# Optimization experiments

Hardware: AMD Instinct MI355X
Metric: run time of the kernel (lower is better)

## Reference

```python
import jax, jax.numpy as jnp
import numpy as np

VOCAB, HIDDEN, BATCH, SEQ = 50000, 256, 64, 2048


def setup_inputs() -> dict:
    key = jax.random.key(0)
    k1, k2, k3, k4 = jax.random.split(key, 4)
    embed = jax.random.normal(k1, (VOCAB, HIDDEN), dtype=jnp.float32) * 0.02
    embed = embed.at[0].set(0.0)  # padding_idx=0
    # orthogonal-ish init approximated by scaled normal; values irrelevant for correctness
    W_x_w = jax.random.normal(k2, (HIDDEN, HIDDEN), dtype=jnp.float32) / np.sqrt(HIDDEN)
    W_x_b = jnp.zeros((HIDDEN,), dtype=jnp.float32)
    W_h_w = jax.random.normal(k3, (HIDDEN, HIDDEN), dtype=jnp.float32) / np.sqrt(HIDDEN)
    x = jax.random.randint(k4, (BATCH, SEQ), 0, VOCAB)
    return {"x": x, "embed": embed, "W_x_w": W_x_w, "W_x_b": W_x_b, "W_h_w": W_h_w}


def reference(x, embed, W_x_w, W_x_b, W_h_w):
    # input projection precomputed for all timesteps: [B, S, H]
    inp = embed[x]                                  # embedding lookup (dropout p=0 is identity)
    x_pre = jnp.einsum('bsd,hd->bsh', inp, W_x_w) + W_x_b
    Wh_t = W_h_w.T                                  # matches torch.mm(h, W_h.weight.t())
    h0 = jnp.zeros((x.shape[0], W_h_w.shape[0]), dtype=x_pre.dtype)

    def step(h, xt):                                # xt: [B, H]
        h = jnp.tanh(xt + h @ Wh_t)
        return h, h

    _, all_states = jax.lax.scan(step, h0, jnp.swapaxes(x_pre, 0, 1))  # [S, B, H]
    return jnp.swapaxes(all_states, 0, 1)           # [B, S, H] (return_all_states=True)
```

## Files before the change

### kernel.cpp

```cpp
#include <hip/hip_runtime.h>
#include <hip/hip_bf16.h>

#define HIDDEN 256
#define BATCH  64
#define SEQ    2048

__global__ __launch_bounds__(256, 4)
void xpre_kernel(const int* __restrict__ x,
                 const float* __restrict__ embed,
                 const float* __restrict__ Wx,
                 const float* __restrict__ bias,
                 float* __restrict__ out) {
    const int tid = threadIdx.x;
    const long row0 = (long)blockIdx.x * 32;

    __shared__ int toks[32];
    if (tid < 32) toks[tid] = x[row0 + tid];
    __syncthreads();

    const float* erow[32];
    #pragma unroll
    for (int r = 0; r < 32; ++r) {
        const int tok = __builtin_amdgcn_readfirstlane(toks[r]);
        erow[r] = embed + (size_t)tok * HIDDEN;
    }

    float acc[32];
    const float bj = bias[tid];
    #pragma unroll
    for (int r = 0; r < 32; ++r) acc[r] = bj;

    const float* wrow = Wx + (size_t)tid * HIDDEN;

    #pragma unroll 4
    for (int d0 = 0; d0 < HIDDEN; d0 += 4) {
        const float4 w = *(const float4*)(wrow + d0);
        #pragma unroll
        for (int r = 0; r < 32; ++r) {
            const float4 ev = *(const float4*)(erow[r] + d0);
            float a = acc[r];
            a = fmaf(w.x, ev.x, a);
            a = fmaf(w.y, ev.y, a);
            a = fmaf(w.z, ev.z, a);
            a = fmaf(w.w, ev.w, a);
            acc[r] = a;
        }
    }

    #pragma unroll
    for (int r = 0; r < 32; ++r) {
        out[(row0 + r) * HIDDEN + tid] = acc[r];
    }
}


#define MAC_ASM(RD) \
  "ds_read_b128 v[48:51], " RD "\n\t" \
  "ds_read_b128 v[52:55], " RD " offset:16\n\t" \
  "ds_read_b128 v[56:59], " RD " offset:32\n\t" \
  "ds_read_b128 v[60:63], " RD " offset:48\n\t" \
  "s_waitcnt lgkmcnt(3)\n\t" \
  "v_pk_mul_f32 v[64:65], v[128:129], v[48:49]\n\t" \
  "v_pk_mul_f32 v[66:67], v[144:145], v[48:49]\n\t" \
  "v_pk_mul_f32 v[68:69], v[160:161], v[48:49]\n\t" \
  "v_pk_mul_f32 v[70:71], v[176:177], v[48:49]\n\t" \
  "v_pk_mul_f32 v[72:73], v[192:193], v[48:49]\n\t" \
  "v_pk_mul_f32 v[74:75], v[208:209], v[48:49]\n\t" \
  "v_pk_mul_f32 v[76:77], v[224:225], v[48:49]\n\t" \
  "v_pk_mul_f32 v[78:79], v[240:241], v[48:49]\n\t" \
  "v_pk_fma_f32 v[64:65], v[130:131], v[50:51], v[64:65]\n\t" \
  "v_pk_fma_f32 v[66:67], v[146:147], v[50:51], v[66:67]\n\t" \
  "v_pk_fma_f32 v[68:69], v[162:163], v[50:51], v[68:69]\n\t" \
  "v_pk_fma_f32 v[70:71], v[178:179], v[50:51], v[70:71]\n\t" \
  "v_pk_fma_f32 v[72:73], v[194:195], v[50:51], v[72:73]\n\t" \
  "v_pk_fma_f32 v[74:75], v[210:211], v[50:51], v[74:75]\n\t" \
  "v_pk_fma_f32 v[76:77], v[226:227], v[50:51], v[76:77]\n\t" \
  "v_pk_fma_f32 v[78:79], v[242:243], v[50:51], v[78:79]\n\t" \
  "s_waitcnt lgkmcnt(2)\n\t" \
  "v_pk_fma_f32 v[64:65], v[132:133], v[52:53], v[64:65]\n\t" \
  "v_pk_fma_f32 v[66:67], v[148:149], v[52:53], v[66:67]\n\t" \
  "v_pk_fma_f32 v[68:69], v[164:165], v[52:53], v[68:69]\n\t" \
  "v_pk_fma_f32 v[70:71], v[180:181], v[52:53], v[70:71]\n\t" \
  "v_pk_fma_f32 v[72:73], v[196:197], v[52:53], v[72:73]\n\t" \
  "v_pk_fma_f32 v[74:75], v[212:213], v[52:53], v[74:75]\n\t" \
  "v_pk_fma_f32 v[76:77], v[228:229], v[52:53], v[76:77]\n\t" \
  "v_pk_fma_f32 v[78:79], v[244:245], v[52:53], v[78:79]\n\t" \
  "v_pk_fma_f32 v[64:65], v[134:135], v[54:55], v[64:65]\n\t" \
  "v_pk_fma_f32 v[66:67], v[150:151], v[54:55], v[66:67]\n\t" \
  "v_pk_fma_f32 v[68:69], v[166:167], v[54:55], v[68:69]\n\t" \
  "v_pk_fma_f32 v[70:71], v[182:183], v[54:55], v[70:71]\n\t" \
  "v_pk_fma_f32 v[72:73], v[198:199], v[54:55], v[72:73]\n\t" \
  "v_pk_fma_f32 v[74:75], v[214:215], v[54:55], v[74:75]\n\t" \
  "v_pk_fma_f32 v[76:77], v[230:231], v[54:55], v[76:77]\n\t" \
  "v_pk_fma_f32 v[78:79], v[246:247], v[54:55], v[78:79]\n\t" \
  "s_waitcnt lgkmcnt(1)\n\t" \
  "v_pk_fma_f32 v[64:65], v[136:137], v[56:57], v[64:65]\n\t" \
  "v_pk_fma_f32 v[66:67], v[152:153], v[56:57], v[66:67]\n\t" \
  "v_pk_fma_f32 v[68:69], v[168:169], v[56:57], v[68:69]\n\t" \
  "v_pk_fma_f32 v[70:71], v[184:185], v[56:57], v[70:71]\n\t" \
  "v_pk_fma_f32 v[72:73], v[200:201], v[56:57], v[72:73]\n\t" \
  "v_pk_fma_f32 v[74:75], v[216:217], v[56:57], v[74:75]\n\t" \
  "v_pk_fma_f32 v[76:77], v[232:233], v[56:57], v[76:77]\n\t" \
  "v_pk_fma_f32 v[78:79], v[248:249], v[56:57], v[78:79]\n\t" \
  "v_pk_fma_f32 v[64:65], v[138:139], v[58:59], v[64:65]\n\t" \
  "v_pk_fma_f32 v[66:67], v[154:155], v[58:59], v[66:67]\n\t" \
  "v_pk_fma_f32 v[68:69], v[170:171], v[58:59], v[68:69]\n\t" \
  "v_pk_fma_f32 v[70:71], v[186:187], v[58:59], v[70:71]\n\t" \
  "v_pk_fma_f32 v[72:73], v[202:203], v[58:59], v[72:73]\n\t" \
  "v_pk_fma_f32 v[74:75], v[218:219], v[58:59], v[74:75]\n\t" \
  "v_pk_fma_f32 v[76:77], v[234:235], v[58:59], v[76:77]\n\t" \
  "v_pk_fma_f32 v[78:79], v[250:251], v[58:59], v[78:79]\n\t" \
  "s_waitcnt lgkmcnt(0)\n\t" \
  "v_pk_fma_f32 v[64:65], v[140:141], v[60:61], v[64:65]\n\t" \
  "v_pk_fma_f32 v[66:67], v[156:157], v[60:61], v[66:67]\n\t" \
  "v_pk_fma_f32 v[68:69], v[172:173], v[60:61], v[68:69]\n\t" \
  "v_pk_fma_f32 v[70:71], v[188:189], v[60:61], v[70:71]\n\t" \
  "v_pk_fma_f32 v[72:73], v[204:205], v[60:61], v[72:73]\n\t" \
  "v_pk_fma_f32 v[74:75], v[220:221], v[60:61], v[74:75]\n\t" \
  "v_pk_fma_f32 v[76:77], v[236:237], v[60:61], v[76:77]\n\t" \
  "v_pk_fma_f32 v[78:79], v[252:253], v[60:61], v[78:79]\n\t" \
  "v_pk_fma_f32 v[64:65], v[142:143], v[62:63], v[64:65]\n\t" \
  "v_pk_fma_f32 v[66:67], v[158:159], v[62:63], v[66:67]\n\t" \
  "v_pk_fma_f32 v[68:69], v[174:175], v[62:63], v[68:69]\n\t" \
  "v_pk_fma_f32 v[70:71], v[190:191], v[62:63], v[70:71]\n\t" \
  "v_pk_fma_f32 v[72:73], v[206:207], v[62:63], v[72:73]\n\t" \
  "v_pk_fma_f32 v[74:75], v[222:223], v[62:63], v[74:75]\n\t" \
  "v_pk_fma_f32 v[76:77], v[238:239], v[62:63], v[76:77]\n\t" \
  "v_pk_fma_f32 v[78:79], v[254:255], v[62:63], v[78:79]\n\t" \
  "v_add_f32 v80, v64, v65\n\t" \
  "v_add_f32 v81, v66, v67\n\t" \
  "v_add_f32 v82, v68, v69\n\t" \
  "v_add_f32 v83, v70, v71\n\t" \
  "v_add_f32 v84, v72, v73\n\t" \
  "v_add_f32 v85, v74, v75\n\t" \
  "v_add_f32 v86, v76, v77\n\t" \
  "v_add_f32 v87, v78, v79\n\t"

#define RED_ASM \
  "v_add_f32_dpp v80, v80, v80 row_ror:8 row_mask:0xf bank_mask:0xf\n\t" \
  "v_add_f32_dpp v81, v81, v81 row_ror:8 row_mask:0xf bank_mask:0xf\n\t" \
  "v_add_f32_dpp v82, v82, v82 row_ror:8 row_mask:0xf bank_mask:0xf\n\t" \
  "v_add_f32_dpp v83, v83, v83 row_ror:8 row_mask:0xf bank_mask:0xf\n\t" \
  "v_add_f32_dpp v84, v84, v84 row_ror:8 row_mask:0xf bank_mask:0xf\n\t" \
  "v_add_f32_dpp v85, v85, v85 row_ror:8 row_mask:0xf bank_mask:0xf\n\t" \
  "v_add_f32_dpp v86, v86, v86 row_ror:8 row_mask:0xf bank_mask:0xf\n\t" \
  "v_add_f32_dpp v87, v87, v87 row_ror:8 row_mask:0xf bank_mask:0xf\n\t" \
  "v_cndmask_b32 v88, v81, v80, s[24:25]\n\t" \
  "v_cndmask_b32 v89, v83, v82, s[24:25]\n\t" \
  "v_cndmask_b32 v90, v85, v84, s[24:25]\n\t" \
  "v_cndmask_b32 v91, v87, v86, s[24:25]\n\t" \
  "v_cndmask_b32 v80, v80, v81, s[24:25]\n\t" \
  "v_cndmask_b32 v82, v82, v83, s[24:25]\n\t" \
  "v_cndmask_b32 v84, v84, v85, s[24:25]\n\t" \
  "v_cndmask_b32 v86, v86, v87, s[24:25]\n\t" \
  "v_add_f32_dpp v80, v88, v80 quad_perm:[1,0,3,2] row_mask:0xf bank_mask:0xf\n\t" \
  "v_add_f32_dpp v82, v89, v82 quad_perm:[1,0,3,2] row_mask:0xf bank_mask:0xf\n\t" \
  "v_add_f32_dpp v84, v90, v84 quad_perm:[1,0,3,2] row_mask:0xf bank_mask:0xf\n\t" \
  "v_add_f32_dpp v86, v91, v86 quad_perm:[1,0,3,2] row_mask:0xf bank_mask:0xf\n\t" \
  "v_cndmask_b32 v88, v82, v80, s[26:27]\n\t" \
  "v_cndmask_b32 v89, v86, v84, s[26:27]\n\t" \
  "v_cndmask_b32 v80, v80, v82, s[26:27]\n\t" \
  "v_cndmask_b32 v84, v84, v86, s[26:27]\n\t" \
  "s_nop 1\n\t" \
  "v_add_f32_dpp v80, v88, v80 quad_perm:[2,3,0,1] row_mask:0xf bank_mask:0xf\n\t" \
  "v_add_f32_dpp v84, v89, v84 quad_perm:[2,3,0,1] row_mask:0xf bank_mask:0xf\n\t" \
  "v_cndmask_b32 v88, v84, v80, s[28:29]\n\t" \
  "v_cndmask_b32 v80, v80, v84, s[28:29]\n\t" \
  "s_nop 1\n\t" \
  "v_add_f32_dpp v80, v88, v80 row_ror:4 row_mask:0xf bank_mask:0xf\n\t"

#define FIN_ASM(WR, XP, MD, MS) \
  "s_waitcnt vmcnt(2)\n\t" \
  "v_add_f32 v99, v80, " XP "\n\t" \
  "v_mul_f32 v93, 0x4038AA3B, v99\n\t" \
  "v_exp_f32 v94, v93\n\t" \
  "s_nop 0\n\t" \
  "v_add_f32 v94, 1.0, v94\n\t" \
  "v_rcp_f32 v95, v94\n\t" \
  "s_nop 0\n\t" \
  "v_fma_f32 v99, -2.0, v95, v96\n\t" \
  "s_and_saveexec_b64 s[20:21], s[22:23]\n\t" \
  "ds_write_b32 " WR ", v99\n\t" \
  "global_store_dword v[100:101], v99, off offset:-2048\n\t" \
  "s_mov_b64 exec, s[20:21]\n\t" \
  "v_mov_b32 " MD ", " MS "\n\t" \
  "v_add_co_u32 v100, vcc, 0x400, v100\n\t" \
  "v_addc_co_u32 v101, vcc, v101, 0, vcc\n\t" \
  "s_waitcnt lgkmcnt(0)\n\t" \
  "s_barrier\n\t"

__global__ __attribute__((amdgpu_flat_work_group_size(512, 512)))
void rnn_scan_kernel(const float* __restrict__ Wh,
                     float* __restrict__ out) {
    const int tid = threadIdx.x;
    const int o   = tid & 15;
    const int pc  = tid >> 4;
    const int b   = blockIdx.x;

    __shared__ __align__(16) float hraw[1024];
    hraw[tid] = 0.0f; hraw[tid + 512] = 0.0f;
    __syncthreads();

    unsigned lbase = (unsigned)(unsigned long long)
                     (__attribute__((address_space(3))) char*)hraw;
    const int col  = pc + 32 * (o & 7);
    const int slot = col + 4 * (col >> 4);
    const unsigned rda = lbase + 80u * (unsigned)o;
    const unsigned rdb = rda + 2048u;
    const unsigned wra = lbase + 2048u + 4u * (unsigned)slot;
    const unsigned wrb = wra - 2048u;

    const float* xa = out + ((size_t)b * SEQ + 2) * HIDDEN + col;
    const unsigned xlo = (unsigned)(size_t)xa;
    const unsigned xhi = (unsigned)((size_t)xa >> 32);

    const float* wp0 = Wh + (size_t)(pc +   0) * HIDDEN + 16 * o;
    const float* wp1 = Wh + (size_t)(pc +  32) * HIDDEN + 16 * o;
    const float* wp2 = Wh + (size_t)(pc +  64) * HIDDEN + 16 * o;
    const float* wp3 = Wh + (size_t)(pc +  96) * HIDDEN + 16 * o;
    const float* wp4 = Wh + (size_t)(pc + 128) * HIDDEN + 16 * o;
    const float* wp5 = Wh + (size_t)(pc + 160) * HIDDEN + 16 * o;
    const float* wp6 = Wh + (size_t)(pc + 192) * HIDDEN + 16 * o;
    const float* wp7 = Wh + (size_t)(pc + 224) * HIDDEN + 16 * o;

    asm volatile(
        "v_mov_b32 v100, %[xlo]\n\t"
        "v_mov_b32 v101, %[xhi]\n\t"
        "v_mov_b32 v96, 1.0\n\t"
        "global_load_dwordx4 v[128:131], %[wp0], off\n\t"
        "global_load_dwordx4 v[132:135], %[wp0], off offset:16\n\t"
        "global_load_dwordx4 v[136:139], %[wp0], off offset:32\n\t"
        "global_load_dwordx4 v[140:143], %[wp0], off offset:48\n\t"
        "global_load_dwordx4 v[144:147], %[wp1], off\n\t"
        "global_load_dwordx4 v[148:151], %[wp1], off offset:16\n\t"
        "global_load_dwordx4 v[152:155], %[wp1], off offset:32\n\t"
        "global_load_dwordx4 v[156:159], %[wp1], off offset:48\n\t"
        "global_load_dwordx4 v[160:163], %[wp2], off\n\t"
        "global_load_dwordx4 v[164:167], %[wp2], off offset:16\n\t"
        "global_load_dwordx4 v[168:171], %[wp2], off offset:32\n\t"
        "global_load_dwordx4 v[172:175], %[wp2], off offset:48\n\t"
        "global_load_dwordx4 v[176:179], %[wp3], off\n\t"
        "global_load_dwordx4 v[180:183], %[wp3], off offset:16\n\t"
        "global_load_dwordx4 v[184:187], %[wp3], off offset:32\n\t"
        "global_load_dwordx4 v[188:191], %[wp3], off offset:48\n\t"
        "global_load_dwordx4 v[192:195], %[wp4], off\n\t"
        "global_load_dwordx4 v[196:199], %[wp4], off offset:16\n\t"
        "global_load_dwordx4 v[200:203], %[wp4], off offset:32\n\t"
        "global_load_dwordx4 v[204:207], %[wp4], off offset:48\n\t"
        "global_load_dwordx4 v[208:211], %[wp5], off\n\t"
        "global_load_dwordx4 v[212:215], %[wp5], off offset:16\n\t"
        "global_load_dwordx4 v[216:219], %[wp5], off offset:32\n\t"
        "global_load_dwordx4 v[220:223], %[wp5], off offset:48\n\t"
        "global_load_dwordx4 v[224:227], %[wp6], off\n\t"
        "global_load_dwordx4 v[228:231], %[wp6], off offset:16\n\t"
        "global_load_dwordx4 v[232:235], %[wp6], off offset:32\n\t"
        "global_load_dwordx4 v[236:239], %[wp6], off offset:48\n\t"
        "global_load_dwordx4 v[240:243], %[wp7], off\n\t"
        "global_load_dwordx4 v[244:247], %[wp7], off offset:16\n\t"
        "global_load_dwordx4 v[248:251], %[wp7], off offset:32\n\t"
        "global_load_dwordx4 v[252:255], %[wp7], off offset:48\n\t"
        "global_load_dword v97,  v[100:101], off offset:-2048\n\t"
        "global_load_dword v103, v[100:101], off offset:-1024\n\t"
        "v_and_b32 v88, 1, %[vo]\n\t"
        "v_cmp_eq_u32 s[24:25], 1, v88\n\t"
        "v_and_b32 v88, 2, %[vo]\n\t"
        "v_cmp_eq_u32 s[26:27], 2, v88\n\t"
        "v_and_b32 v88, 4, %[vo]\n\t"
        "v_cmp_eq_u32 s[28:29], 4, v88\n\t"
        "v_cmp_gt_u32 s[22:23], 8, %[vo]\n\t"
        "s_movk_i32 s30, 0x400\n\t"
        "s_waitcnt vmcnt(0)\n\t"
        "RNN%=:\n\t"
        "s_cmp_eq_u32 s30, 1\n\t"
        "s_cbranch_scc1 LDA%=\n\t"
        "global_load_dword v102, v[100:101], off\n\t"
        "s_branch LCA%=\n\t"
        "LDA%=:\n\t"
        "global_load_dword v102, v[100:101], off offset:-1024\n\t"
        "LCA%=:\n\t"
        MAC_ASM("%[rda]")
        RED_ASM
        FIN_ASM("%[wra]", "v97", "v98", "v103")
        "s_cmp_eq_u32 s30, 1\n\t"
        "s_cbranch_scc1 LDB%=\n\t"
        "global_load_dword v103, v[100:101], off\n\t"
        "s_branch LCB%=\n\t"
        "LDB%=:\n\t"
        "global_load_dword v103, v[100:101], off offset:-2048\n\t"
        "LCB%=:\n\t"
        MAC_ASM("%[rdb]")
        RED_ASM
        FIN_ASM("%[wrb]", "v98", "v97", "v102")
        "s_sub_u32 s30, s30, 1\n\t"
        "s_cmp_lg_u32 s30, 0\n\t"
        "s_cbranch_scc1 RNN%=\n\t"
        "s_waitcnt vmcnt(0) lgkmcnt(0)\n\t"
        :
        : [wp0] "v"(wp0), [wp1] "v"(wp1), [wp2] "v"(wp2), [wp3] "v"(wp3),
          [wp4] "v"(wp4), [wp5] "v"(wp5), [wp6] "v"(wp6), [wp7] "v"(wp7),
          [xlo] "v"(xlo), [xhi] "v"(xhi),
          [rda] "v"(rda), [rdb] "v"(rdb), [wra] "v"(wra), [wrb] "v"(wrb),
          [vo]  "v"(o)
        : "memory", "vcc", "scc",
          "s20","s21","s22","s23","s24","s25","s26","s27","s28","s29","s30",
          "v48","v49","v50","v51","v52","v53","v54","v55",
          "v56","v57","v58","v59","v60","v61","v62","v63",
          "v64","v65","v66","v67","v68","v69","v70","v71",
          "v72","v73","v74","v75","v76","v77","v78","v79",
          "v80","v81","v82","v83","v84","v85","v86","v87",
          "v88","v89","v90","v91","v92","v93","v94","v95",
          "v96","v97","v98","v99","v100","v101","v102","v103",
          "v104","v105","v106","v107","v108","v109","v110","v111",
          "v112","v113","v114","v115","v116","v117","v118","v119",
          "v120","v121","v122","v123","v124","v125","v126","v127",
          "v128","v129","v130","v131","v132","v133","v134","v135",
          "v136","v137","v138","v139","v140","v141","v142","v143",
          "v144","v145","v146","v147","v148","v149","v150","v151",
          "v152","v153","v154","v155","v156","v157","v158","v159",
          "v160","v161","v162","v163","v164","v165","v166","v167",
          "v168","v169","v170","v171","v172","v173","v174","v175",
          "v176","v177","v178","v179","v180","v181","v182","v183",
          "v184","v185","v186","v187","v188","v189","v190","v191",
          "v192","v193","v194","v195","v196","v197","v198","v199",
          "v200","v201","v202","v203","v204","v205","v206","v207",
          "v208","v209","v210","v211","v212","v213","v214","v215",
          "v216","v217","v218","v219","v220","v221","v222","v223",
          "v224","v225","v226","v227","v228","v229","v230","v231",
          "v232","v233","v234","v235","v236","v237","v238","v239",
          "v240","v241","v242","v243","v244","v245","v246","v247",
          "v248","v249","v250","v251","v252","v253","v254","v255");
}

extern "C" void kernel_launch(void* const* d_in, const int* in_sizes, int n_in,
                              void* d_out, int out_size, void* d_ws, size_t ws_size,
                              hipStream_t stream) {
    const int*   x     = (const int*)d_in[0];
    const float* embed = (const float*)d_in[1];
    const float* Wx    = (const float*)d_in[2];
    const float* Wxb   = (const float*)d_in[3];
    const float* Wh    = (const float*)d_in[4];
    float* out = (float*)d_out;

    const int nrows = BATCH * SEQ;
    xpre_kernel<<<nrows / 32, 256, 0, stream>>>(x, embed, Wx, Wxb, out);

    rnn_scan_kernel<<<BATCH, 512, 0, stream>>>(Wh, out);
}
```

Measured before the change: 1.703 ms.

## Stage embedding rows in LDS and register-tile xpre over rows and columns

New measurement: 1.986 ms. +16.6%, slower.

```diff
diff --git a/kernel.cpp b/kernel.cpp
--- a/kernel.cpp
+++ b/kernel.cpp
@@ -12,44 +12,72 @@
                  const float* __restrict__ bias,
                  float* __restrict__ out) {
     const int tid = threadIdx.x;
+    const int rg  = tid >> 6;
+    const int j   = tid & 63;
     const long row0 = (long)blockIdx.x * 32;
 
     __shared__ int toks[32];
+    __shared__ __align__(16) float e[32][HIDDEN];
+
     if (tid < 32) toks[tid] = x[row0 + tid];
     __syncthreads();
 
-    const float* erow[32];
     #pragma unroll
     for (int r = 0; r < 32; ++r) {
-        const int tok = __builtin_amdgcn_readfirstlane(toks[r]);
-        erow[r] = embed + (size_t)tok * HIDDEN;
+        e[r][tid] = embed[(long)toks[r] * HIDDEN + tid];
     }
-
-    float acc[32];
-    const float bj = bias[tid];
+    __syncthreads();
+
+    const float* wr0 = Wx + (size_t)(j      ) * HIDDEN;
+    const float* wr1 = Wx + (size_t)(j +  64) * HIDDEN;
+    const float* wr2 = Wx + (size_t)(j + 128) * HIDDEN;
+    const float* wr3 = Wx + (size_t)(j + 192) * HIDDEN;
+
+    float a0[8], a1[8], a2[8], a3[8];
+    const float b0 = bias[j];
+    const float b1 = bias[j + 64];
+    const float b2 = bias[j + 128];
+    const float b3 = bias[j + 192];
     #pragma unroll
-    for (int r = 0; r < 32; ++r) acc[r] = bj;
-
-    const float* wrow = Wx + (size_t)tid * HIDDEN;
-
-    #pragma unroll 4
+    for (int r = 0; r < 8; ++r) { a0[r] = b0; a1[r] = b1; a2[r] = b2; a3[r] = b3; }
+
+    const int rbase = rg << 3;
+
+    #pragma unroll 2
     for (int d0 = 0; d0 < HIDDEN; d0 += 4) {
-        const float4 w = *(const float4*)(wrow + d0);
+        const float4 w0 = *(const float4*)(wr0 + d0);
+        const float4 w1 = *(const float4*)(wr1 + d0);
+        const float4 w2 = *(const float4*)(wr2 + d0);
+        const float4 w3 = *(const float4*)(wr3 + d0);
         #pragma unroll
-        for (int r = 0; r < 32; ++r) {
-            const float4 ev = *(const float4*)(erow[r] + d0);
-            float a = acc[r];
-            a = fmaf(w.x, ev.x, a);
-            a = fmaf(w.y, ev.y, a);
-            a = fmaf(w.z, ev.z, a);
-            a = fmaf(w.w, ev.w, a);
-            acc[r] = a;
+        for (int r = 0; r < 8; ++r) {
+            const float4 ev = *(const float4*)&e[rbase + r][d0];
+            float t0 = a0[r];
+            t0 = fmaf(w0.x, ev.x, t0); t0 = fmaf(w0.y, ev.y, t0);
+            t0 = fmaf(w0.z, ev.z, t0); t0 = fmaf(w0.w, ev.w, t0);
+            a0[r] = t0;
+            float t1 = a1[r];
+            t1 = fmaf(w1.x, ev.x, t1); t1 = fmaf(w1.y, ev.y, t1);
+            t1 = fmaf(w1.z, ev.z, t1); t1 = fmaf(w1.w, ev.w, t1);
+            a1[r] = t1;
+            float t2 = a2[r];
+            t2 = fmaf(w2.x, ev.x, t2); t2 = fmaf(w2.y, ev.y, t2);
+            t2 = fmaf(w2.z, ev.z, t2); t2 = fmaf(w2.w, ev.w, t2);
+            a2[r] = t2;
+            float t3 = a3[r];
+            t3 = fmaf(w3.x, ev.x, t3); t3 = fmaf(w3.y, ev.y, t3);
+            t3 = fmaf(w3.z, ev.z, t3); t3 = fmaf(w3.w, ev.w, t3);
+            a3[r] = t3;
         }
     }
 
     #pragma unroll
-    for (int r = 0; r < 32; ++r) {
-        out[(row0 + r) * HIDDEN + tid] = acc[r];
+    for (int r = 0; r < 8; ++r) {
+        const size_t orow = (size_t)(row0 + rbase + r) * HIDDEN;
+        out[orow + j]       = a0[r];
+        out[orow + j + 64]  = a1[r];
+        out[orow + j + 128] = a2[r];
+        out[orow + j + 192] = a3[r];
     }
 }
 
```
